# Performance work log

Measured on AMD Instinct MI355X. Metric: run time of the kernel, lower is better.

Reference implementation:

```python
import jax, jax.numpy as jnp
import numpy as np

NH, DH, DHR = 16, 128, 64  # heads, head dim, decoupled rope dim
ROPE_BASE = 10000.0

def _rope(x):
    # x: (B, L, H, Dr) with Dr even; interleaved-pair RoPE (torchtune style)
    B, L, H, Dr = x.shape
    pos = jnp.arange(L, dtype=jnp.float32)
    inv_freq = 1.0 / (ROPE_BASE ** (jnp.arange(0, Dr, 2, dtype=jnp.float32) / Dr))
    ang = pos[:, None] * inv_freq[None, :]          # (L, Dr/2)
    cos = jnp.cos(ang)[None, :, None, :].astype(x.dtype)
    sin = jnp.sin(ang)[None, :, None, :].astype(x.dtype)
    x1, x2 = x[..., 0::2], x[..., 1::2]
    out = jnp.stack([x1 * cos - x2 * sin, x1 * sin + x2 * cos], axis=-1)
    return out.reshape(B, L, H, Dr)

def setup_inputs() -> dict:
    key = jax.random.key(0)
    ks = jax.random.split(key, 9)
    s = 0.02
    return {
        'x':     jax.random.normal(ks[0], (2, 2048, 2048), jnp.float32),
        'W_DKV': jax.random.normal(ks[1], (2048, 682), jnp.float32) * s,
        'W_UK':  jax.random.normal(ks[2], (682, 2048), jnp.float32) * s,
        'W_UV':  jax.random.normal(ks[3], (682, 2048), jnp.float32) * s,
        'W_KR':  jax.random.normal(ks[4], (2048, 64), jnp.float32) * s,
        'W_DQ':  jax.random.normal(ks[5], (2048, 682), jnp.float32) * s,
        'W_UQ':  jax.random.normal(ks[6], (682, 2048), jnp.float32) * s,
        'W_QR':  jax.random.normal(ks[7], (682, 1024), jnp.float32) * s,
        'W_O':   jax.random.normal(ks[8], (2048, 2048), jnp.float32) * s,
    }

def reference(x, W_DKV, W_UK, W_UV, W_KR, W_DQ, W_UQ, W_QR, W_O):
    B, L, D = x.shape
    # --- KV path ---
    c_KV = x @ W_DKV                                   # (B, L, dc)
    k_C = (c_KV @ W_UK).reshape(B, L, NH, DH)          # content keys
    k_R = _rope((x @ W_KR).reshape(B, L, 1, DHR))      # shared rope key head
    k_R = jnp.broadcast_to(k_R, (B, L, NH, DHR))
    k = jnp.concatenate([k_C, k_R], axis=-1)           # (B, L, NH, DH+DHR)
    v = (c_KV @ W_UV).reshape(B, L, NH, DH)
    # --- Q path ---
    c_Q = x @ W_DQ                                     # (B, L, dc')
    q_C = (c_Q @ W_UQ).reshape(B, L, NH, DH)
    q_R = _rope((c_Q @ W_QR).reshape(B, L, NH, DHR))
    q = jnp.concatenate([q_C, q_R], axis=-1)           # (B, L, NH, DH+DHR)
    # --- attention (causal) ---
    scale = 1.0 / jnp.sqrt(jnp.float32(DH + DHR))
    scores = jnp.einsum('blhd,bmhd->bhlm', q, k) * scale
    causal = jnp.tril(jnp.ones((L, L), dtype=bool))
    scores = jnp.where(causal[None, None], scores, jnp.finfo(scores.dtype).min)
    attn = jax.nn.softmax(scores, axis=-1)
    o = jnp.einsum('bhlm,bmhd->blhd', attn, v).reshape(B, L, NH * DH)
    return o @ W_O
```

## Files before the change

kernel.cpp:

```cpp
#include <hip/hip_runtime.h>
#include <stdint.h>

typedef __attribute__((ext_vector_type(8))) __bf16 bf16x8;
typedef __attribute__((ext_vector_type(4))) float f32x4;

#define DEVI static __device__ __forceinline__

DEVI uint16_t f2b(float f) {
  uint32_t u = __float_as_uint(f);
  u += 0x7FFFu + ((u >> 16) & 1u);
  return (uint16_t)(u >> 16);
}
DEVI float b2f(uint16_t b) { return __uint_as_float(((uint32_t)b) << 16); }

DEVI void gl_lds16(const void* g, void* l) {
  __builtin_amdgcn_global_load_lds((const __attribute__((address_space(1))) void*)g,
                                   (__attribute__((address_space(3))) void*)l, 16, 0, 0);
}

DEVI f32x4 mfma16(bf16x8 a, bf16x8 b, f32x4 c) {
  return __builtin_amdgcn_mfma_f32_16x16x32_bf16(a, b, c, 0, 0, 0);
}

#define BARX asm volatile("s_barrier" ::: "memory")
#define WLG0 asm volatile("s_waitcnt lgkmcnt(0)" ::: "memory")
#define WV4 asm volatile("s_waitcnt vmcnt(4)" ::: "memory")
#define PRIO1 __builtin_amdgcn_s_setprio(1)
#define PRIO0 __builtin_amdgcn_s_setprio(0)

static constexpr size_t OFF_XB = 0;
static constexpr size_t OFF_WD = 8388608;
static constexpr size_t OFF_WUKV = OFF_WD + 3670016;
static constexpr size_t OFF_WUQR = OFF_WUKV + 3145728;
static constexpr size_t OFF_WO = OFF_WUQR + 2359296;
static constexpr size_t OFF_CD = OFF_WO + 4194304;
static constexpr size_t OFF_CUKV = OFF_CD + 7340032;
static constexpr size_t OFF_CUQR = OFF_CUKV + 16777216;
static constexpr size_t OFF_VT = OFF_CUQR + 12582912;

__global__ void pre_kernel(const float* __restrict__ x, const float* __restrict__ Wdkv,
                           const float* __restrict__ Wuk, const float* __restrict__ Wuv,
                           const float* __restrict__ Wkr, const float* __restrict__ Wdq,
                           const float* __restrict__ Wuq, const float* __restrict__ Wqr,
                           const float* __restrict__ Wo, uint16_t* __restrict__ ws) {
  const int bid = blockIdx.x;
  const int t = threadIdx.x;
  if (bid >= 3264) {
    int id = (bid - 3264) * 256 + t;
    float4 v = ((const float4*)x)[id];
    uint16_t o[4] = {f2b(v.x), f2b(v.y), f2b(v.z), f2b(v.w)};
    *(uint64_t*)&ws[OFF_XB + (size_t)id * 4] = *(uint64_t*)o;
    return;
  }
  const float* W;
  uint16_t* Wt;
  int Kw, Nw, Kp, nx, rb;
  if (bid < 384) {
    W = Wdkv; Wt = ws + OFF_WD; Kw = 2048; Nw = 682; Kp = 2048; nx = 12; rb = bid;
  } else if (bid < 768) {
    W = Wdq; Wt = ws + OFF_WD + (size_t)768 * 2048; Kw = 2048; Nw = 682; Kp = 2048; nx = 12; rb = bid - 384;
  } else if (bid < 896) {
    W = Wkr; Wt = ws + OFF_WD + (size_t)1536 * 2048; Kw = 2048; Nw = 64; Kp = 2048; nx = 4; rb = bid - 768;
  } else if (bid < 1280) {
    W = Wuk; Wt = ws + OFF_WUKV; Kw = 682; Nw = 2048; Kp = 768; nx = 32; rb = bid - 896;
  } else if (bid < 1664) {
    W = Wuv; Wt = ws + OFF_WUKV + (size_t)2048 * 768; Kw = 682; Nw = 2048; Kp = 768; nx = 32; rb = bid - 1280;
  } else if (bid < 2048) {
    W = Wuq; Wt = ws + OFF_WUQR; Kw = 682; Nw = 2048; Kp = 768; nx = 32; rb = bid - 1664;
  } else if (bid < 2240) {
    W = Wqr; Wt = ws + OFF_WUQR + (size_t)2048 * 768; Kw = 682; Nw = 1024; Kp = 768; nx = 16; rb = bid - 2048;
  } else {
    W = Wo; Wt = ws + OFF_WO; Kw = 2048; Nw = 2048; Kp = 2048; nx = 32; rb = bid - 2240;
  }
  const int n0 = (rb % nx) * 64, k0 = (rb / nx) * 64;
  __shared__ uint16_t T[64][72];
#pragma unroll
  for (int p = 0; p < 2; ++p) {
    int r = p * 32 + (t >> 3);
    int c0 = (t & 7) * 8;
    int gr = k0 + r;
#pragma unroll
    for (int e = 0; e < 8; ++e) {
      int gc = n0 + c0 + e;
      float v = (gr < Kw && gc < Nw) ? W[(size_t)gr * Nw + gc] : 0.f;
      T[c0 + e][r] = f2b(v);
    }
  }
  __syncthreads();
#pragma unroll
  for (int p = 0; p < 2; ++p) {
    int dr = p * 32 + (t >> 3);
    int mc = (t & 7) * 8;
    uint16_t tmp[8];
#pragma unroll
    for (int e = 0; e < 8; ++e) tmp[e] = T[dr][mc + e];
    *(uint64_t*)&Wt[(size_t)(n0 + dr) * Kp + k0 + mc] = ((uint64_t*)tmp)[0];
    *(uint64_t*)&Wt[(size_t)(n0 + dr) * Kp + k0 + mc + 4] = ((uint64_t*)tmp)[1];
  }
}

template <int BM, bool F32OUT>
__global__ __launch_bounds__(512, 1) void gemm8(const uint16_t* __restrict__ A, int lda,
                                                const uint16_t* __restrict__ Bt,
                                                void* __restrict__ Cv, int ldc, int K) {
  constexpr int MF = BM / 32;
  constexpr int MH = MF / 2;
  constexpr int AL = BM / 128;
  constexpr int ABYTES = BM * 128;
  __shared__ char lds[2 * BM * 128 + 2 * 256 * 128];
  char* const LB = lds + 2 * ABYTES;
  const int tid = threadIdx.x;
  const int lane = tid & 63;
  const int lr = lane & 15, lgb = (lane >> 4) * 16;
  const int wid = tid >> 6;
  const int g = wid >> 2;
  const int wc = (wid & 3) * 64;
  const int rA0 = g * (BM / 2) + lr;
  const int rB0 = wc + lr;
  const size_t row0 = (size_t)blockIdx.y * BM, col0 = (size_t)blockIdx.x * 256;
  const char* Agb = (const char*)(A + row0 * lda);
  const char* Btb = (const char*)(Bt + col0 * K);
  const size_t ldab = (size_t)lda * 2;
  const size_t ldbb = (size_t)K * 2;
  const int nk = K >> 6;
  const int ni = nk >> 1;

  f32x4 acc[MF][4] = {};
  bf16x8 aF[MH][2], bF[4][2];

  auto stageA = [&](int kt, int buf, int hf) {
#pragma unroll
    for (int j = 0; j < AL; ++j) {
      int c = j * 512 + tid;
      int cl = c ^ (((c >> 5) & 1) << 1);
      int row = hf * (BM / 2) + (cl >> 3);
      gl_lds16(Agb + (size_t)row * ldab + (size_t)kt * 128 + (cl & 7) * 16,
               lds + buf * ABYTES + hf * (ABYTES / 2) + (j * 512 + (tid & 0x1C0)) * 16);
    }
  };
  auto stageB = [&](int kt, int buf, int hf) {
#pragma unroll
    for (int j = 0; j < 2; ++j) {
      int c = j * 512 + tid;
      int cl = c ^ (((c >> 5) & 1) << 1);
      int row = hf * 128 + (cl >> 3);
      gl_lds16(Btb + (size_t)row * ldbb + (size_t)kt * 128 + (cl & 7) * 16,
               LB + buf * 32768 + hf * 16384 + (j * 512 + (tid & 0x1C0)) * 16);
    }
  };
  auto ldAm = [&](int buf, int mb) {
#pragma unroll
    for (int m = 0; m < MH; ++m) {
      int r = rA0 + (mb + m) * 16;
      int ro = r * 128;
      int sw = ((r >> 2) & 1) << 5;
#pragma unroll
      for (int kk = 0; kk < 2; ++kk)
        aF[m][kk] = *(const bf16x8*)(lds + buf * ABYTES + ((ro + kk * 64 + lgb) ^ sw));
    }
  };
  auto ldBn = [&](int buf, int nb) {
#pragma unroll
    for (int n = 0; n < 2; ++n) {
      int r = rB0 + (nb + n) * 16;
      int ro = r * 128;
      int sw = ((r >> 2) & 1) << 5;
#pragma unroll
      for (int kk = 0; kk < 2; ++kk)
        bF[nb + n][kk] = *(const bf16x8*)(LB + buf * 32768 + ((ro + kk * 64 + lgb) ^ sw));
    }
  };
  auto mmac = [&](int mb, int nb) {
#pragma unroll
    for (int m = 0; m < MH; ++m)
#pragma unroll
      for (int n = 0; n < 2; ++n)
#pragma unroll
        for (int kk = 0; kk < 2; ++kk)
          acc[mb + m][nb + n] = mfma16(aF[m][kk], bF[nb + n][kk], acc[mb + m][nb + n]);
  };

  stageA(0, 0, 0); stageA(0, 0, 1); stageB(0, 0, 0); stageB(0, 0, 1);
  stageB(1, 1, 0); stageB(1, 1, 1);
  WV4; BARX;

  for (int i = 0; i < ni; ++i) {
    const int t1 = 2 * i + 1;
    const int tn = (2 * i + 2 < nk) ? 2 * i + 2 : nk - 1;
    const int tn1 = (2 * i + 3 < nk) ? 2 * i + 3 : nk - 1;
    ldAm(0, 0); ldBn(0, 0); stageA(t1, 1, 0);
    BARX; WLG0; PRIO1; mmac(0, 0); PRIO0; BARX;
    ldBn(0, 2); stageA(t1, 1, 1);
    BARX; WLG0; PRIO1; mmac(0, 2); PRIO0; BARX;
    ldAm(0, MH); stageB(tn, 0, 0);
    BARX; WLG0; PRIO1; mmac(MH, 0); PRIO0; BARX;
    stageB(tn, 0, 1);
    BARX; PRIO1; mmac(MH, 2); PRIO0; WV4; BARX;
    ldAm(1, 0); ldBn(1, 0); stageA(tn, 0, 0);
    BARX; WLG0; PRIO1; mmac(0, 0); PRIO0; BARX;
    ldBn(1, 2); stageA(tn, 0, 1);
    BARX; WLG0; PRIO1; mmac(0, 2); PRIO0; BARX;
    ldAm(1, MH); stageB(tn1, 1, 0);
    BARX; WLG0; PRIO1; mmac(MH, 0); PRIO0; BARX;
    stageB(tn1, 1, 1);
    BARX; PRIO1; mmac(MH, 2); PRIO0; WV4; BARX;
  }
  asm volatile("s_waitcnt vmcnt(0)" ::: "memory");

#pragma unroll
  for (int m = 0; m < MF; ++m)
#pragma unroll
    for (int n = 0; n < 4; ++n)
#pragma unroll
      for (int j = 0; j < 4; ++j) {
        size_t row = row0 + g * (BM / 2) + m * 16 + (lane >> 4) * 4 + j;
        size_t col = col0 + wc + n * 16 + lr;
        if (F32OUT)
          ((float*)Cv)[row * ldc + col] = acc[m][n][j];
        else
          ((uint16_t*)Cv)[row * ldc + col] = f2b(acc[m][n][j]);
      }
}

__global__ __launch_bounds__(512, 1) void gemm8up(const uint16_t* __restrict__ cdA, int lda,
                                                  const uint16_t* __restrict__ wukv,
                                                  const uint16_t* __restrict__ wuqr,
                                                  uint16_t* __restrict__ cukv,
                                                  uint16_t* __restrict__ cuqr, int K) {
  constexpr int BM = 256;
  constexpr int MF = 8, MH = 4, AL = 2;
  constexpr int ABYTES = BM * 128;
  __shared__ char lds[2 * BM * 128 + 2 * 256 * 128];
  char* const LB = lds + 2 * ABYTES;
  const int tid = threadIdx.x;
  const int lane = tid & 63;
  const int lr = lane & 15, lgb = (lane >> 4) * 16;
  const int wid = tid >> 6;
  const int g = wid >> 2;
  const int wc = (wid & 3) * 64;
  const int rA0 = g * (BM / 2) + lr;
  const int rB0 = wc + lr;
  const bool second = blockIdx.x >= 16;
  const int xl = second ? blockIdx.x - 16 : blockIdx.x;
  const uint16_t* A = second ? cdA + 768 : cdA;
  const uint16_t* Bt = second ? wuqr : wukv;
  uint16_t* Cv = second ? cuqr : cukv;
  const int ldc = second ? 3072 : 4096;
  const size_t row0 = (size_t)blockIdx.y * BM, col0 = (size_t)xl * 256;
  const char* Agb = (const char*)(A + row0 * lda);
  const char* Btb = (const char*)(Bt + col0 * K);
  const size_t ldab = (size_t)lda * 2;
  const size_t ldbb = (size_t)K * 2;
  const int nk = K >> 6;
  const int ni = nk >> 1;

  f32x4 acc[MF][4] = {};
  bf16x8 aF[MH][2], bF[4][2];

  auto stageA = [&](int kt, int buf, int hf) {
#pragma unroll
    for (int j = 0; j < AL; ++j) {
      int c = j * 512 + tid;
      int cl = c ^ (((c >> 5) & 1) << 1);
      int row = hf * (BM / 2) + (cl >> 3);
      gl_lds16(Agb + (size_t)row * ldab + (size_t)kt * 128 + (cl & 7) * 16,
               lds + buf * ABYTES + hf * (ABYTES / 2) + (j * 512 + (tid & 0x1C0)) * 16);
    }
  };
  auto stageB = [&](int kt, int buf, int hf) {
#pragma unroll
    for (int j = 0; j < 2; ++j) {
      int c = j * 512 + tid;
      int cl = c ^ (((c >> 5) & 1) << 1);
      int row = hf * 128 + (cl >> 3);
      gl_lds16(Btb + (size_t)row * ldbb + (size_t)kt * 128 + (cl & 7) * 16,
               LB + buf * 32768 + hf * 16384 + (j * 512 + (tid & 0x1C0)) * 16);
    }
  };
  auto ldAm = [&](int buf, int mb) {
#pragma unroll
    for (int m = 0; m < MH; ++m) {
      int r = rA0 + (mb + m) * 16;
      int ro = r * 128;
      int sw = ((r >> 2) & 1) << 5;
#pragma unroll
      for (int kk = 0; kk < 2; ++kk)
        aF[m][kk] = *(const bf16x8*)(lds + buf * ABYTES + ((ro + kk * 64 + lgb) ^ sw));
    }
  };
  auto ldBn = [&](int buf, int nb) {
#pragma unroll
    for (int n = 0; n < 2; ++n) {
      int r = rB0 + (nb + n) * 16;
      int ro = r * 128;
      int sw = ((r >> 2) & 1) << 5;
#pragma unroll
      for (int kk = 0; kk < 2; ++kk)
        bF[nb + n][kk] = *(const bf16x8*)(LB + buf * 32768 + ((ro + kk * 64 + lgb) ^ sw));
    }
  };
  auto mmac = [&](int mb, int nb) {
#pragma unroll
    for (int m = 0; m < MH; ++m)
#pragma unroll
      for (int n = 0; n < 2; ++n)
#pragma unroll
        for (int kk = 0; kk < 2; ++kk)
          acc[mb + m][nb + n] = mfma16(aF[m][kk], bF[nb + n][kk], acc[mb + m][nb + n]);
  };

  stageA(0, 0, 0); stageA(0, 0, 1); stageB(0, 0, 0); stageB(0, 0, 1);
  stageB(1, 1, 0); stageB(1, 1, 1);
  WV4; BARX;

  for (int i = 0; i < ni; ++i) {
    const int t1 = 2 * i + 1;
    const int tn = (2 * i + 2 < nk) ? 2 * i + 2 : nk - 1;
    const int tn1 = (2 * i + 3 < nk) ? 2 * i + 3 : nk - 1;
    ldAm(0, 0); ldBn(0, 0); stageA(t1, 1, 0);
    BARX; WLG0; PRIO1; mmac(0, 0); PRIO0; BARX;
    ldBn(0, 2); stageA(t1, 1, 1);
    BARX; WLG0; PRIO1; mmac(0, 2); PRIO0; BARX;
    ldAm(0, MH); stageB(tn, 0, 0);
    BARX; WLG0; PRIO1; mmac(MH, 0); PRIO0; BARX;
    stageB(tn, 0, 1);
    BARX; PRIO1; mmac(MH, 2); PRIO0; WV4; BARX;
    ldAm(1, 0); ldBn(1, 0); stageA(tn, 0, 0);
    BARX; WLG0; PRIO1; mmac(0, 0); PRIO0; BARX;
    ldBn(1, 2); stageA(tn, 0, 1);
    BARX; WLG0; PRIO1; mmac(0, 2); PRIO0; BARX;
    ldAm(1, MH); stageB(tn1, 1, 0);
    BARX; WLG0; PRIO1; mmac(MH, 0); PRIO0; BARX;
    stageB(tn1, 1, 1);
    BARX; PRIO1; mmac(MH, 2); PRIO0; WV4; BARX;
  }
  asm volatile("s_waitcnt vmcnt(0)" ::: "memory");

#pragma unroll
  for (int m = 0; m < MF; ++m)
#pragma unroll
    for (int n = 0; n < 4; ++n)
#pragma unroll
      for (int j = 0; j < 4; ++j) {
        size_t row = row0 + g * (BM / 2) + m * 16 + (lane >> 4) * 4 + j;
        size_t col = col0 + wc + n * 16 + lr;
        Cv[row * ldc + col] = f2b(acc[m][n][j]);
      }
}

__global__ void misc_kernel(uint16_t* __restrict__ cd, uint16_t* __restrict__ cuqr,
                            const uint16_t* __restrict__ cukv, uint16_t* __restrict__ vt) {
  const int bid = blockIdx.x;
  const int t = threadIdx.x;
  if (bid < 512) {
    int id = bid * 256 + t;
    int row = id >> 5, i = id & 31;
    int pos = row & 2047;
    float invf = exp2f(-13.287712379549449f * (float)i / 32.f);
    float ang = (float)pos * invf;
    float s, c;
    sincosf(ang, &s, &c);
    size_t base = (size_t)row * 1792 + 1536 + 2 * i;
    float x1 = b2f(cd[base]), x2 = b2f(cd[base + 1]);
    cd[base] = f2b(x1 * c - x2 * s);
    cd[base + 1] = f2b(x1 * s + x2 * c);
    return;
  }
  if (bid < 8704) {
    int id = (bid - 512) * 256 + t;
    int row = id >> 9;
    int rem = id & 511;
    int h = rem >> 5, i = rem & 31;
    int pos = row & 2047;
    float invf = exp2f(-13.287712379549449f * (float)i / 32.f);
    float ang = (float)pos * invf;
    float s, c;
    sincosf(ang, &s, &c);
    size_t base = (size_t)row * 3072 + 2048 + h * 64 + 2 * i;
    float x1 = b2f(cuqr[base]), x2 = b2f(cuqr[base + 1]);
    cuqr[base] = f2b(x1 * c - x2 * s);
    cuqr[base + 1] = f2b(x1 * s + x2 * c);
    return;
  }
  const int idx = bid - 8704;
  const int mt = idx & 31, dt = (idx >> 5) & 1, bh = idx >> 6;
  const int b = bh >> 4, h = bh & 15;
  const int m0 = mt * 64, d0 = dt * 64;
  __shared__ uint16_t T[64][72];
#pragma unroll
  for (int p = 0; p < 2; ++p) {
    int r = p * 32 + (t >> 3), c8 = (t & 7) * 8;
    const uint16_t* s = &cukv[((size_t)(b * 2048 + m0 + r)) * 4096 + 2048 + h * 128 + d0 + c8];
    uint16_t tmp[8];
    ((uint64_t*)tmp)[0] = ((const uint64_t*)s)[0];
    ((uint64_t*)tmp)[1] = ((const uint64_t*)s)[1];
#pragma unroll
    for (int e = 0; e < 8; ++e) T[c8 + e][r] = tmp[e];
  }
  __syncthreads();
#pragma unroll
  for (int p = 0; p < 2; ++p) {
    int dr = p * 32 + (t >> 3), mc = (t & 7) * 8;
    uint16_t tmp[8];
#pragma unroll
    for (int e = 0; e < 8; ++e) tmp[e] = T[dr][mc + e];
    uint16_t* dstp = &vt[((size_t)(bh * 128 + d0 + dr)) * 2048 + m0 + mc];
    ((uint64_t*)dstp)[0] = ((uint64_t*)tmp)[0];
    ((uint64_t*)dstp)[1] = ((uint64_t*)tmp)[1];
  }
}

__global__ __launch_bounds__(512, 1) void attn_kernel(const uint16_t* __restrict__ cuqr,
                                                      const uint16_t* __restrict__ cukv,
                                                      const uint16_t* __restrict__ cd,
                                                      const uint16_t* __restrict__ vt,
                                                      uint16_t* __restrict__ obuf) {
  __shared__ uint16_t Ks[2][64 * 192];
  __shared__ uint16_t Vs[2][128 * 64];
  __shared__ uint16_t Ps[8 * 16 * 64];
  const int tid = threadIdx.x;
  const int wid = tid >> 6, lane = tid & 63;
  const int lr = lane & 15, lg = lane >> 4;
  const int bid = blockIdx.x;
  const int wg = (bid & 7) * 32 + (bid >> 3);
  const int pairi = wg & 7;
  const int bh = wg >> 3;
  const int b = bh >> 4, h = bh & 15;
  const float sc2 = 0.07216878364870323f * 1.4426950408889634f;

  const char* Kcb = (const char*)cukv + (size_t)b * 2048 * 8192 + h * 256;
  const char* Krb = (const char*)cd + (size_t)b * 2048 * 3584 + 3072;
  const char* Vb = (const char*)vt + (size_t)bh * 524288;
  char* const Ks0 = (char*)Ks[0];
  char* const Vs0 = (char*)Vs[0];
  char* PwB = (char*)(Ps + wid * 1024);

  const char* kbase[3];
  size_t kstep[3];
  int klds[3];
#pragma unroll
  for (int i = 0; i < 3; ++i) {
    int c = i * 512 + tid;
    int r = c / 24, c16 = c % 24;
    klds[i] = r * 384 + ((c16 * 16) ^ ((r & 7) << 4));
    if (c16 < 16) {
      kbase[i] = Kcb + (size_t)r * 8192 + c16 * 16;
      kstep[i] = (size_t)64 * 8192;
    } else {
      kbase[i] = Krb + (size_t)r * 3584 + (c16 - 16) * 16;
      kstep[i] = (size_t)64 * 3584;
    }
  }
  const char* vbase[2];
  int vlds[2];
#pragma unroll
  for (int i = 0; i < 2; ++i) {
    int c = i * 512 + tid;
    int d = c >> 3, c16 = c & 7;
    vlds[i] = d * 128 + ((c16 * 16) ^ ((d & 7) << 4));
    vbase[i] = Vb + (size_t)d * 4096 + c16 * 16;
  }

  for (int ph = 0; ph < 2; ++ph) {
    const int qt = ph ? (15 - pairi) : pairi;
    const int q0 = qt * 128;
    const int nt = 2 * (qt + 1);
    const int qrow = q0 + wid * 16 + lr;
    bf16x8 qf[6];
    {
      const char* Qcp = (const char*)cuqr + (size_t)(b * 2048 + qrow) * 6144 + h * 256 + lg * 16;
      const char* Qrp =
          (const char*)cuqr + (size_t)(b * 2048 + qrow) * 6144 + 4096 + h * 128 + lg * 16;
#pragma unroll
      for (int kb = 0; kb < 4; ++kb) qf[kb] = *(const bf16x8*)(Qcp + kb * 64);
#pragma unroll
      for (int kb = 0; kb < 2; ++kb) qf[4 + kb] = *(const bf16x8*)(Qrp + kb * 64);
    }
    f32x4 o[8] = {};
    float mrun[4], lrun[4];
#pragma unroll
    for (int j = 0; j < 4; ++j) { mrun[j] = -INFINITY; lrun[j] = 0.f; }

    const char* kp[3];
    const char* vp[2];
    bf16x8 kreg[3], vreg[2];
#pragma unroll
    for (int i = 0; i < 3; ++i) kp[i] = kbase[i];
#pragma unroll
    for (int i = 0; i < 2; ++i) vp[i] = vbase[i];
#pragma unroll
    for (int i = 0; i < 3; ++i) { kreg[i] = *(const bf16x8*)kp[i]; kp[i] += kstep[i]; }
#pragma unroll
    for (int i = 0; i < 2; ++i) { vreg[i] = *(const bf16x8*)vp[i]; vp[i] += 128; }
#pragma unroll
    for (int i = 0; i < 3; ++i) *(bf16x8*)(Ks0 + klds[i]) = kreg[i];
#pragma unroll
    for (int i = 0; i < 2; ++i) *(bf16x8*)(Vs0 + vlds[i]) = vreg[i];
    __syncthreads();

    for (int t = 0; t < nt; ++t) {
      const bool more = (t + 1 < nt);
      if (more) {
#pragma unroll
        for (int i = 0; i < 3; ++i) { kreg[i] = *(const bf16x8*)kp[i]; kp[i] += kstep[i]; }
#pragma unroll
        for (int i = 0; i < 2; ++i) { vreg[i] = *(const bf16x8*)vp[i]; vp[i] += 128; }
      }
      const int cb = t & 1;
      const char* KsB = Ks0 + cb * 24576;
      const char* VsB = Vs0 + cb * 16384;
      if (t * 64 <= q0 + wid * 16 + 15) {
        f32x4 s[4] = {};
        __builtin_amdgcn_s_setprio(1);
#pragma unroll
        for (int n = 0; n < 4; ++n) {
          int r = n * 16 + lr;
          const char* kptr = KsB + r * 384;
          int sw = (r & 7) << 4;
#pragma unroll
          for (int kb = 0; kb < 6; ++kb)
            s[n] = mfma16(qf[kb], *(const bf16x8*)(kptr + ((kb * 64 + lg * 16) ^ sw)), s[n]);
        }
        __builtin_amdgcn_s_setprio(0);
        if (t * 64 + 63 > q0 + wid * 16) {
#pragma unroll
          for (int n = 0; n < 4; ++n)
#pragma unroll
            for (int j = 0; j < 4; ++j)
              if (t * 64 + n * 16 + lr > q0 + wid * 16 + lg * 4 + j) s[n][j] = -INFINITY;
        }
        float pm[4];
#pragma unroll
        for (int j = 0; j < 4; ++j) {
          float v = fmaxf(fmaxf(s[0][j], s[1][j]), fmaxf(s[2][j], s[3][j]));
          v = fmaxf(v, __shfl_xor(v, 1));
          v = fmaxf(v, __shfl_xor(v, 2));
          v = fmaxf(v, __shfl_xor(v, 4));
          v = fmaxf(v, __shfl_xor(v, 8));
          pm[j] = v;
        }
        bool exceed = false;
#pragma unroll
        for (int j = 0; j < 4; ++j) exceed |= (pm[j] > mrun[j] + 76.8f);
        if (__any(exceed)) {
          float alpha[4];
#pragma unroll
          for (int j = 0; j < 4; ++j) {
            float mn = fmaxf(mrun[j], pm[j]);
            alpha[j] = exp2f((mrun[j] - mn) * sc2);
            mrun[j] = mn;
            lrun[j] *= alpha[j];
          }
#pragma unroll
          for (int n2 = 0; n2 < 8; ++n2)
#pragma unroll
            for (int j = 0; j < 4; ++j) o[n2][j] *= alpha[j];
        }
        float rs[4] = {0.f, 0.f, 0.f, 0.f};
#pragma unroll
        for (int n = 0; n < 4; ++n)
#pragma unroll
          for (int j = 0; j < 4; ++j) {
            float p = exp2f((s[n][j] - mrun[j]) * sc2);
            rs[j] += p;
            int row = lg * 4 + j;
            *(uint16_t*)(PwB + row * 128 + ((((n * 16 + lr)) * 2) ^ ((row & 7) << 4))) = f2b(p);
          }
#pragma unroll
        for (int j = 0; j < 4; ++j) lrun[j] += rs[j];
        __builtin_amdgcn_s_setprio(1);
#pragma unroll
        for (int kb2 = 0; kb2 < 2; ++kb2) {
          bf16x8 pa = *(const bf16x8*)(PwB + lr * 128 + ((kb2 * 64 + lg * 16) ^ ((lr & 7) << 4)));
#pragma unroll
          for (int n2 = 0; n2 < 8; ++n2) {
            int vr = n2 * 16 + lr;
            o[n2] = mfma16(
                pa, *(const bf16x8*)(VsB + vr * 128 + ((kb2 * 64 + lg * 16) ^ ((vr & 7) << 4))),
                o[n2]);
          }
        }
        __builtin_amdgcn_s_setprio(0);
      }
      if (more) {
        char* KsN = Ks0 + (cb ^ 1) * 24576;
        char* VsN = Vs0 + (cb ^ 1) * 16384;
#pragma unroll
        for (int i = 0; i < 3; ++i) *(bf16x8*)(KsN + klds[i]) = kreg[i];
#pragma unroll
        for (int i = 0; i < 2; ++i) *(bf16x8*)(VsN + vlds[i]) = vreg[i];
      }
      __syncthreads();
    }
#pragma unroll
    for (int j = 0; j < 4; ++j) {
      float v = lrun[j];
      v += __shfl_xor(v, 1);
      v += __shfl_xor(v, 2);
      v += __shfl_xor(v, 4);
      v += __shfl_xor(v, 8);
      lrun[j] = v;
    }
    float inv[4];
#pragma unroll
    for (int j = 0; j < 4; ++j) inv[j] = 1.f / lrun[j];
#pragma unroll
    for (int n2 = 0; n2 < 8; ++n2)
#pragma unroll
      for (int j = 0; j < 4; ++j) {
        size_t row = (size_t)b * 2048 + q0 + wid * 16 + lg * 4 + j;
        size_t col = (size_t)h * 128 + n2 * 16 + lr;
        obuf[row * 2048 + col] = f2b(o[n2][j] * inv[j]);
      }
  }
}

extern "C" void kernel_launch(void* const* d_in, const int* in_sizes, int n_in,
                              void* d_out, int out_size, void* d_ws, size_t ws_size,
                              hipStream_t stream) {
  (void)in_sizes; (void)n_in; (void)out_size; (void)ws_size;
  const float* x = (const float*)d_in[0];
  const float* Wdkv = (const float*)d_in[1];
  const float* Wuk = (const float*)d_in[2];
  const float* Wuv = (const float*)d_in[3];
  const float* Wkr = (const float*)d_in[4];
  const float* Wdq = (const float*)d_in[5];
  const float* Wuq = (const float*)d_in[6];
  const float* Wqr = (const float*)d_in[7];
  const float* Wo = (const float*)d_in[8];
  uint16_t* ws = (uint16_t*)d_ws;

  uint16_t* xb = ws + OFF_XB;
  uint16_t* obuf = ws + OFF_XB;
  uint16_t* wd = ws + OFF_WD;
  uint16_t* wukv = ws + OFF_WUKV;
  uint16_t* wuqr = ws + OFF_WUQR;
  uint16_t* wo = ws + OFF_WO;
  uint16_t* cd = ws + OFF_CD;
  uint16_t* cukv = ws + OFF_CUKV;
  uint16_t* cuqr = ws + OFF_CUQR;
  uint16_t* vtb = ws + OFF_VT;

  pre_kernel<<<11456, 256, 0, stream>>>(x, Wdkv, Wuk, Wuv, Wkr, Wdq, Wuq, Wqr, Wo, ws);
  gemm8<128, false><<<dim3(7, 32), 512, 0, stream>>>(xb, 2048, wd, cd, 1792, 2048);
  gemm8up<<<dim3(28, 16), 512, 0, stream>>>(cd, 1792, wukv, wuqr, cukv, cuqr, 768);
  misc_kernel<<<10752, 256, 0, stream>>>(cd, cuqr, cukv, vtb);
  attn_kernel<<<256, 512, 0, stream>>>(cuqr, cukv, cd, vtb, obuf);
  gemm8<128, true><<<dim3(8, 32), 512, 0, stream>>>(obuf, 2048, wo, d_out, 2048, 2048);
}
```

Baseline: 263.3 us.

## Split paired attention tiles into separate blocks and single-buffer V for two blocks/CU

The attention kernel previously processed two query tiles (a light and heavy causal pair) sequentially per block with 256 blocks. Now each block handles a single query tile with 512 blocks, launch bounds allow two blocks per CU, and V shared memory is single-buffered to fit LDS for two resident blocks. V writes move after an extra barrier, adding a second sync per iteration; the intent is higher occupancy and latency hiding at the cost of register pressure limits and an extra barrier.

New measurement: 297.2 us. 1.13x slower.

```diff
diff --git a/kernel.cpp b/kernel.cpp
--- a/kernel.cpp
+++ b/kernel.cpp
@@ -410,21 +410,23 @@
   }
 }
 
-__global__ __launch_bounds__(512, 1) void attn_kernel(const uint16_t* __restrict__ cuqr,
+__global__ __launch_bounds__(512, 2) void attn_kernel(const uint16_t* __restrict__ cuqr,
                                                       const uint16_t* __restrict__ cukv,
                                                       const uint16_t* __restrict__ cd,
                                                       const uint16_t* __restrict__ vt,
                                                       uint16_t* __restrict__ obuf) {
   __shared__ uint16_t Ks[2][64 * 192];
-  __shared__ uint16_t Vs[2][128 * 64];
+  __shared__ uint16_t Vs[128 * 64];
   __shared__ uint16_t Ps[8 * 16 * 64];
   const int tid = threadIdx.x;
   const int wid = tid >> 6, lane = tid & 63;
   const int lr = lane & 15, lg = lane >> 4;
   const int bid = blockIdx.x;
-  const int wg = (bid & 7) * 32 + (bid >> 3);
-  const int pairi = wg & 7;
-  const int bh = wg >> 3;
+  const int cpair = bid >> 8, r0 = bid & 255;
+  const int rp = (r0 & 7) * 32 + (r0 >> 3);
+  const int bh = rp >> 3;
+  const int qtl = rp & 7;
+  const int qt = cpair ? (15 - qtl) : qtl;
   const int b = bh >> 4, h = bh & 15;
   const float sc2 = 0.07216878364870323f * 1.4426950408889634f;
 
@@ -432,187 +434,179 @@
   const char* Krb = (const char*)cd + (size_t)b * 2048 * 3584 + 3072;
   const char* Vb = (const char*)vt + (size_t)bh * 524288;
   char* const Ks0 = (char*)Ks[0];
-  char* const Vs0 = (char*)Vs[0];
+  char* const VsB = (char*)Vs;
   char* PwB = (char*)(Ps + wid * 1024);
 
-  const char* kbase[3];
+  const char* kp[3];
   size_t kstep[3];
   int klds[3];
 #pragma unroll
   for (int i = 0; i < 3; ++i) {
     int c = i * 512 + tid;
-    int r = c / 24, c16 = c % 24;
-    klds[i] = r * 384 + ((c16 * 16) ^ ((r & 7) << 4));
+    int rr = c / 24, c16 = c % 24;
+    klds[i] = rr * 384 + ((c16 * 16) ^ ((rr & 7) << 4));
     if (c16 < 16) {
-      kbase[i] = Kcb + (size_t)r * 8192 + c16 * 16;
+      kp[i] = Kcb + (size_t)rr * 8192 + c16 * 16;
       kstep[i] = (size_t)64 * 8192;
     } else {
-      kbase[i] = Krb + (size_t)r * 3584 + (c16 - 16) * 16;
+      kp[i] = Krb + (size_t)rr * 3584 + (c16 - 16) * 16;
       kstep[i] = (size_t)64 * 3584;
     }
   }
-  const char* vbase[2];
+  const char* vp[2];
   int vlds[2];
 #pragma unroll
   for (int i = 0; i < 2; ++i) {
     int c = i * 512 + tid;
     int d = c >> 3, c16 = c & 7;
     vlds[i] = d * 128 + ((c16 * 16) ^ ((d & 7) << 4));
-    vbase[i] = Vb + (size_t)d * 4096 + c16 * 16;
-  }
-
-  for (int ph = 0; ph < 2; ++ph) {
-    const int qt = ph ? (15 - pairi) : pairi;
-    const int q0 = qt * 128;
-    const int nt = 2 * (qt + 1);
-    const int qrow = q0 + wid * 16 + lr;
-    bf16x8 qf[6];
-    {
-      const char* Qcp = (const char*)cuqr + (size_t)(b * 2048 + qrow) * 6144 + h * 256 + lg * 16;
-      const char* Qrp =
-          (const char*)cuqr + (size_t)(b * 2048 + qrow) * 6144 + 4096 + h * 128 + lg * 16;
-#pragma unroll
-      for (int kb = 0; kb < 4; ++kb) qf[kb] = *(const bf16x8*)(Qcp + kb * 64);
-#pragma unroll
-      for (int kb = 0; kb < 2; ++kb) qf[4 + kb] = *(const bf16x8*)(Qrp + kb * 64);
-    }
-    f32x4 o[8] = {};
-    float mrun[4], lrun[4];
-#pragma unroll
-    for (int j = 0; j < 4; ++j) { mrun[j] = -INFINITY; lrun[j] = 0.f; }
-
-    const char* kp[3];
-    const char* vp[2];
-    bf16x8 kreg[3], vreg[2];
-#pragma unroll
-    for (int i = 0; i < 3; ++i) kp[i] = kbase[i];
-#pragma unroll
-    for (int i = 0; i < 2; ++i) vp[i] = vbase[i];
-#pragma unroll
-    for (int i = 0; i < 3; ++i) { kreg[i] = *(const bf16x8*)kp[i]; kp[i] += kstep[i]; }
-#pragma unroll
-    for (int i = 0; i < 2; ++i) { vreg[i] = *(const bf16x8*)vp[i]; vp[i] += 128; }
-#pragma unroll
-    for (int i = 0; i < 3; ++i) *(bf16x8*)(Ks0 + klds[i]) = kreg[i];
-#pragma unroll
-    for (int i = 0; i < 2; ++i) *(bf16x8*)(Vs0 + vlds[i]) = vreg[i];
+    vp[i] = Vb + (size_t)d * 4096 + c16 * 16;
+  }
+
+  const int q0 = qt * 128;
+  const int nt = 2 * (qt + 1);
+  const int qrow = q0 + wid * 16 + lr;
+  bf16x8 qf[6];
+  {
+    const char* Qcp = (const char*)cuqr + (size_t)(b * 2048 + qrow) * 6144 + h * 256 + lg * 16;
+    const char* Qrp =
+        (const char*)cuqr + (size_t)(b * 2048 + qrow) * 6144 + 4096 + h * 128 + lg * 16;
+#pragma unroll
+    for (int kb = 0; kb < 4; ++kb) qf[kb] = *(const bf16x8*)(Qcp + kb * 64);
+#pragma unroll
+    for (int kb = 0; kb < 2; ++kb) qf[4 + kb] = *(const bf16x8*)(Qrp + kb * 64);
+  }
+  f32x4 o[8] = {};
+  float mrun[4], lrun[4];
+#pragma unroll
+  for (int j = 0; j < 4; ++j) { mrun[j] = -INFINITY; lrun[j] = 0.f; }
+
+  bf16x8 kreg[3], vreg[2];
+#pragma unroll
+  for (int i = 0; i < 3; ++i) { kreg[i] = *(const bf16x8*)kp[i]; kp[i] += kstep[i]; }
+#pragma unroll
+  for (int i = 0; i < 2; ++i) { vreg[i] = *(const bf16x8*)vp[i]; vp[i] += 128; }
+#pragma unroll
+  for (int i = 0; i < 3; ++i) *(bf16x8*)(Ks0 + klds[i]) = kreg[i];
+#pragma unroll
+  for (int i = 0; i < 2; ++i) *(bf16x8*)(VsB + vlds[i]) = vreg[i];
+  __syncthreads();
+
+  for (int t = 0; t < nt; ++t) {
+    const bool more = (t + 1 < nt);
+    if (more) {
+#pragma unroll
+      for (int i = 0; i < 3; ++i) { kreg[i] = *(const bf16x8*)kp[i]; kp[i] += kstep[i]; }
+#pragma unroll
+      for (int i = 0; i < 2; ++i) { vreg[i] = *(const bf16x8*)vp[i]; vp[i] += 128; }
+    }
+    const int cb = t & 1;
+    const char* KsB = Ks0 + cb * 24576;
+    if (t * 64 <= q0 + wid * 16 + 15) {
+      f32x4 s[4] = {};
+      __builtin_amdgcn_s_setprio(1);
+#pragma unroll
+      for (int n = 0; n < 4; ++n) {
+        int rr = n * 16 + lr;
+        const char* kptr = KsB + rr * 384;
+        int sw = (rr & 7) << 4;
+#pragma unroll
+        for (int kb = 0; kb < 6; ++kb)
+          s[n] = mfma16(qf[kb], *(const bf16x8*)(kptr + ((kb * 64 + lg * 16) ^ sw)), s[n]);
+      }
+      __builtin_amdgcn_s_setprio(0);
+      if (t * 64 + 63 > q0 + wid * 16) {
+#pragma unroll
+        for (int n = 0; n < 4; ++n)
+#pragma unroll
+          for (int j = 0; j < 4; ++j)
+            if (t * 64 + n * 16 + lr > q0 + wid * 16 + lg * 4 + j) s[n][j] = -INFINITY;
+      }
+      float pm[4];
+#pragma unroll
+      for (int j = 0; j < 4; ++j) {
+        float v = fmaxf(fmaxf(s[0][j], s[1][j]), fmaxf(s[2][j], s[3][j]));
+        v = fmaxf(v, __shfl_xor(v, 1));
+        v = fmaxf(v, __shfl_xor(v, 2));
+        v = fmaxf(v, __shfl_xor(v, 4));
+        v = fmaxf(v, __shfl_xor(v, 8));
+        pm[j] = v;
+      }
+      bool exceed = false;
+#pragma unroll
+      for (int j = 0; j < 4; ++j) exceed |= (pm[j] > mrun[j] + 76.8f);
+      if (__any(exceed)) {
+        float alpha[4];
+#pragma unroll
+        for (int j = 0; j < 4; ++j) {
+          float mn = fmaxf(mrun[j], pm[j]);
+          alpha[j] = exp2f((mrun[j] - mn) * sc2);
+          mrun[j] = mn;
+          lrun[j] *= alpha[j];
+        }
+#pragma unroll
+        for (int n2 = 0; n2 < 8; ++n2)
+#pragma unroll
+          for (int j = 0; j < 4; ++j) o[n2][j] *= alpha[j];
+      }
+      float rs[4] = {0.f, 0.f, 0.f, 0.f};
+#pragma unroll
+      for (int n = 0; n < 4; ++n)
+#pragma unroll
+        for (int j = 0; j < 4; ++j) {
+          float p = exp2f((s[n][j] - mrun[j]) * sc2);
+          rs[j] += p;
+          int row = lg * 4 + j;
+          *(uint16_t*)(PwB + row * 128 + ((((n * 16 + lr)) * 2) ^ ((row & 7) << 4))) = f2b(p);
+        }
+#pragma unroll
+      for (int j = 0; j < 4; ++j) lrun[j] += rs[j];
+      __builtin_amdgcn_s_setprio(1);
+#pragma unroll
+      for (int kb2 = 0; kb2 < 2; ++kb2) {
+        bf16x8 pa = *(const bf16x8*)(PwB + lr * 128 + ((kb2 * 64 + lg * 16) ^ ((lr & 7) << 4)));
+#pragma unroll
+        for (int n2 = 0; n2 < 8; ++n2) {
+          int vr = n2 * 16 + lr;
+          o[n2] = mfma16(
+              pa, *(const bf16x8*)(VsB + vr * 128 + ((kb2 * 64 + lg * 16) ^ ((vr & 7) << 4))),
+              o[n2]);
+        }
+      }
+      __builtin_amdgcn_s_setprio(0);
+    }
+    if (more) {
+      char* KsN = Ks0 + (cb ^ 1) * 24576;
+#pragma unroll
+      for (int i = 0; i < 3; ++i) *(bf16x8*)(KsN + klds[i]) = kreg[i];
+    }
     __syncthreads();
-
-    for (int t = 0; t < nt; ++t) {
-      const bool more = (t + 1 < nt);
-      if (more) {
-#pragma unroll
-        for (int i = 0; i < 3; ++i) { kreg[i] = *(const bf16x8*)kp[i]; kp[i] += kstep[i]; }
-#pragma unroll
-        for (int i = 0; i < 2; ++i) { vreg[i] = *(const bf16x8*)vp[i]; vp[i] += 128; }
-      }
-      const int cb = t & 1;
-      const char* KsB = Ks0 + cb * 24576;
-      const char* VsB = Vs0 + cb * 16384;
-      if (t * 64 <= q0 + wid * 16 + 15) {
-        f32x4 s[4] = {};
-        __builtin_amdgcn_s_setprio(1);
-#pragma unroll
-        for (int n = 0; n < 4; ++n) {
-          int r = n * 16 + lr;
-          const char* kptr = KsB + r * 384;
-          int sw = (r & 7) << 4;
-#pragma unroll
-          for (int kb = 0; kb < 6; ++kb)
-            s[n] = mfma16(qf[kb], *(const bf16x8*)(kptr + ((kb * 64 + lg * 16) ^ sw)), s[n]);
-        }
-        __builtin_amdgcn_s_setprio(0);
-        if (t * 64 + 63 > q0 + wid * 16) {
-#pragma unroll
-          for (int n = 0; n < 4; ++n)
-#pragma unroll
-            for (int j = 0; j < 4; ++j)
-              if (t * 64 + n * 16 + lr > q0 + wid * 16 + lg * 4 + j) s[n][j] = -INFINITY;
-        }
-        float pm[4];
-#pragma unroll
-        for (int j = 0; j < 4; ++j) {
-          float v = fmaxf(fmaxf(s[0][j], s[1][j]), fmaxf(s[2][j], s[3][j]));
-          v = fmaxf(v, __shfl_xor(v, 1));
-          v = fmaxf(v, __shfl_xor(v, 2));
-          v = fmaxf(v, __shfl_xor(v, 4));
-          v = fmaxf(v, __shfl_xor(v, 8));
-          pm[j] = v;
-        }
-        bool exceed = false;
-#pragma unroll
-        for (int j = 0; j < 4; ++j) exceed |= (pm[j] > mrun[j] + 76.8f);
-        if (__any(exceed)) {
-          float alpha[4];
-#pragma unroll
-          for (int j = 0; j < 4; ++j) {
-            float mn = fmaxf(mrun[j], pm[j]);
-            alpha[j] = exp2f((mrun[j] - mn) * sc2);
-            mrun[j] = mn;
-            lrun[j] *= alpha[j];
-          }
-#pragma unroll
-          for (int n2 = 0; n2 < 8; ++n2)
-#pragma unroll
-            for (int j = 0; j < 4; ++j) o[n2][j] *= alpha[j];
-        }
-        float rs[4] = {0.f, 0.f, 0.f, 0.f};
-#pragma unroll
-        for (int n = 0; n < 4; ++n)
-#pragma unroll
-          for (int j = 0; j < 4; ++j) {
-            float p = exp2f((s[n][j] - mrun[j]) * sc2);
-            rs[j] += p;
-            int row = lg * 4 + j;
-            *(uint16_t*)(PwB + row * 128 + ((((n * 16 + lr)) * 2) ^ ((row & 7) << 4))) = f2b(p);
-          }
-#pragma unroll
-        for (int j = 0; j < 4; ++j) lrun[j] += rs[j];
-        __builtin_amdgcn_s_setprio(1);
-#pragma unroll
-        for (int kb2 = 0; kb2 < 2; ++kb2) {
-          bf16x8 pa = *(const bf16x8*)(PwB + lr * 128 + ((kb2 * 64 + lg * 16) ^ ((lr & 7) << 4)));
-#pragma unroll
-          for (int n2 = 0; n2 < 8; ++n2) {
-            int vr = n2 * 16 + lr;
-            o[n2] = mfma16(
-                pa, *(const bf16x8*)(VsB + vr * 128 + ((kb2 * 64 + lg * 16) ^ ((vr & 7) << 4))),
-                o[n2]);
-          }
-        }
-        __builtin_amdgcn_s_setprio(0);
-      }
-      if (more) {
-        char* KsN = Ks0 + (cb ^ 1) * 24576;
-        char* VsN = Vs0 + (cb ^ 1) * 16384;
-#pragma unroll
-        for (int i = 0; i < 3; ++i) *(bf16x8*)(KsN + klds[i]) = kreg[i];
-#pragma unroll
-        for (int i = 0; i < 2; ++i) *(bf16x8*)(VsN + vlds[i]) = vreg[i];
-      }
-      __syncthreads();
-    }
+    if (more) {
+#pragma unroll
+      for (int i = 0; i < 2; ++i) *(bf16x8*)(VsB + vlds[i]) = vreg[i];
+    }
+    __syncthreads();
+  }
+#pragma unroll
+  for (int j = 0; j < 4; ++j) {
+    float v = lrun[j];
+    v += __shfl_xor(v, 1);
+    v += __shfl_xor(v, 2);
+    v += __shfl_xor(v, 4);
+    v += __shfl_xor(v, 8);
+    lrun[j] = v;
+  }
+  float inv[4];
+#pragma unroll
+  for (int j = 0; j < 4; ++j) inv[j] = 1.f / lrun[j];
+#pragma unroll
+  for (int n2 = 0; n2 < 8; ++n2)
 #pragma unroll
     for (int j = 0; j < 4; ++j) {
-      float v = lrun[j];
-      v += __shfl_xor(v, 1);
-      v += __shfl_xor(v, 2);
-      v += __shfl_xor(v, 4);
-      v += __shfl_xor(v, 8);
-      lrun[j] = v;
-    }
-    float inv[4];
-#pragma unroll
-    for (int j = 0; j < 4; ++j) inv[j] = 1.f / lrun[j];
-#pragma unroll
-    for (int n2 = 0; n2 < 8; ++n2)
-#pragma unroll
-      for (int j = 0; j < 4; ++j) {
-        size_t row = (size_t)b * 2048 + q0 + wid * 16 + lg * 4 + j;
-        size_t col = (size_t)h * 128 + n2 * 16 + lr;
-        obuf[row * 2048 + col] = f2b(o[n2][j] * inv[j]);
-      }
-  }
+      size_t row = (size_t)b * 2048 + q0 + wid * 16 + lg * 4 + j;
+      size_t col = (size_t)h * 128 + n2 * 16 + lr;
+      obuf[row * 2048 + col] = f2b(o[n2][j] * inv[j]);
+    }
 }
 
 extern "C" void kernel_launch(void* const* d_in, const int* in_sizes, int n_in,
@@ -645,6 +639,6 @@
   gemm8<128, false><<<dim3(7, 32), 512, 0, stream>>>(xb, 2048, wd, cd, 1792, 2048);
   gemm8up<<<dim3(28, 16), 512, 0, stream>>>(cd, 1792, wukv, wuqr, cukv, cuqr, 768);
   misc_kernel<<<10752, 256, 0, stream>>>(cd, cuqr, cukv, vtb);
-  attn_kernel<<<256, 512, 0, stream>>>(cuqr, cukv, cd, vtb, obuf);
+  attn_kernel<<<512, 512, 0, stream>>>(cuqr, cukv, cd, vtb, obuf);
   gemm8<128, true><<<dim3(8, 32), 512, 0, stream>>>(obuf, 2048, wo, d_out, 2048, 2048);
 }
```
